# Kernel optimization log

Hardware: AMD Instinct MI355X
Metric: run time of the kernel (lower is better)

Reference implementation:

```python
import jax, jax.numpy as jnp
import numpy as np

EPS = 1e-5
TEMP = 3.0
MASK_FILL = 1e-4


def _conv2d(x, w, b):
    # x: [N,C,H,W], w: [O,C,kh,kw], stride 1, padding 1
    y = jax.lax.conv_general_dilated(x, w, (1, 1), [(1, 1), (1, 1)],
                                     dimension_numbers=('NCHW', 'OIHW', 'NCHW'))
    return y + b[None, :, None, None]


def _cp_conv4d(x, w1, b1, w2, b2):
    # CenterPivotConv4d: 2D conv over (ha,wa) per (hb,wb) + 2D conv over (hb,wb) per (ha,wa)
    B, C, ha, wa, hb, wb = x.shape
    O = w1.shape[0]
    x1 = x.transpose(0, 4, 5, 1, 2, 3).reshape(B * hb * wb, C, ha, wa)
    o1 = _conv2d(x1, w1, b1).reshape(B, hb, wb, O, ha, wa).transpose(0, 3, 4, 5, 1, 2)
    x2 = x.transpose(0, 2, 3, 1, 4, 5).reshape(B * ha * wa, C, hb, wb)
    o2 = _conv2d(x2, w2, b2).reshape(B, ha, wa, O, hb, wb).transpose(0, 3, 1, 2, 4, 5)
    return o1 + o2


def _mutual_matching(c):
    # c: [B,ch,fs1,fs2,fs3,fs4]; corr * (corr/maxA) * (corr/maxB)
    mA = jnp.max(c, axis=(4, 5), keepdims=True)  # max over (fs3*fs4)
    mB = jnp.max(c, axis=(2, 3), keepdims=True)  # max over (fs1*fs2)
    return c * (c / (mA + EPS)) * (c / (mB + EPS))


def _neigh_consensus(x, params):
    def stack(y):
        for (w1, b1, w2, b2) in params:
            y = jax.nn.relu(_cp_conv4d(y, w1, b1, w2, b2))
        return y
    # symmetric mode: conv(x) + conv(x with pairs swapped) swapped back
    xp = x.transpose(0, 1, 4, 5, 2, 3)
    return stack(x) + stack(xp).transpose(0, 1, 4, 5, 2, 3)


def setup_inputs() -> dict:
    key = jax.random.key(0)
    ks = jax.random.split(key, 16)
    B, S, Cv = 4, 32, 256
    corr = jax.random.normal(ks[0], (B, S, S, S, S), dtype=jnp.float32)
    v = jax.random.normal(ks[1], (B, Cv, S * S), dtype=jnp.float32)
    ig_mask = jax.random.randint(ks[2], (B, S * S), 0, 2) > 0
    layer_io = [(1, 10), (10, 10), (10, 1)]
    inp = {'corr': corr, 'v': v, 'ig_mask': ig_mask}
    for i, (ci, co) in enumerate(layer_io):
        k1, k2 = jax.random.split(ks[3 + i])
        inp[f'l{i}_w1'] = jax.random.normal(k1, (co, ci, 3, 3), dtype=jnp.float32) * 0.1
        inp[f'l{i}_b1'] = jnp.zeros((co,), dtype=jnp.float32)
        inp[f'l{i}_w2'] = jax.random.normal(k2, (co, ci, 3, 3), dtype=jnp.float32) * 0.1
        inp[f'l{i}_b2'] = jnp.zeros((co,), dtype=jnp.float32)
    return inp


def reference(corr, v, ig_mask,
              l0_w1, l0_b1, l0_w2, l0_b2,
              l1_w1, l1_b1, l1_w2, l1_b2,
              l2_w1, l2_b1, l2_w2, l2_b2):
    params = [(l0_w1, l0_b1, l0_w2, l0_b2),
              (l1_w1, l1_b1, l1_w2, l1_b2),
              (l2_w1, l2_b1, l2_w2, l2_b2)]
    B, h, w, hs, ws = corr.shape
    c = corr[:, None]                      # [B,1,h,w,hs,ws]
    c = _mutual_matching(c)
    c = _neigh_consensus(c, params)
    c = _mutual_matching(c)
    corr2d = c.reshape(B, h * w, hs * ws)
    corr2d = jnp.where(ig_mask[:, None, :], MASK_FILL, corr2d)
    attn = jax.nn.softmax(corr2d * TEMP, axis=-1)  # [B, hw, hsws]
    weighted_v = jnp.einsum('bcs,bqs->bcq', v, attn)
    return weighted_v.reshape(B, -1, h, w)
```

## Files before the change

kernel.cpp:

```cpp
#include <hip/hip_runtime.h>
#include <math.h>

#define BN 4
#define HW 1024
#define SP 1024

static constexpr float EPS = 1e-5f;
static constexpr float TEMPF = 3.0f;
static constexpr float MASK_FILL = 1e-4f;
static constexpr size_t CH1 = (size_t)HW * SP;
static constexpr size_t CH10 = (size_t)10 * HW * SP;

__device__ __forceinline__ float wave_max(float v) {
    for (int o = 32; o; o >>= 1) v = fmaxf(v, __shfl_xor(v, o));
    return v;
}
__device__ __forceinline__ float wave_sum(float v) {
    for (int o = 32; o; o >>= 1) v += __shfl_xor(v, o);
    return v;
}
__device__ __forceinline__ float block_max(float v, float* red) {
    v = wave_max(v);
    int w = threadIdx.x >> 6;
    if ((threadIdx.x & 63) == 0) red[w] = v;
    __syncthreads();
    v = fmaxf(fmaxf(red[0], red[1]), fmaxf(red[2], red[3]));
    __syncthreads();
    return v;
}
__device__ __forceinline__ float block_sum(float v, float* red) {
    v = wave_sum(v);
    int w = threadIdx.x >> 6;
    if ((threadIdx.x & 63) == 0) red[w] = v;
    __syncthreads();
    v = red[0] + red[1] + red[2] + red[3];
    __syncthreads();
    return v;
}

__global__ void wt_prep(const float* __restrict__ l0w1, const float* __restrict__ l0w2,
                        const float* __restrict__ l1w1, const float* __restrict__ l1w2,
                        const float* __restrict__ l2w1, const float* __restrict__ l2w2,
                        float* __restrict__ wt) {
    int t = threadIdx.x;
    for (int i = t; i < 90; i += 256) {
        int co = i % 10, tap = i / 10;
        wt[tap * 20 + co] = l0w1[co * 9 + tap];
        wt[tap * 20 + 10 + co] = l0w2[co * 9 + tap];
    }
    for (int i = t; i < 900; i += 256) {
        int co = i % 10, tap = (i / 10) % 9, ci = i / 90;
        wt[180 + ci * 180 + tap * 20 + co] = l1w1[(co * 10 + ci) * 9 + tap];
        wt[180 + ci * 180 + tap * 20 + 10 + co] = l1w2[(co * 10 + ci) * 9 + tap];
    }
    for (int i = t; i < 90; i += 256) {
        int tap = i % 9, ci = i / 9;
        wt[1980 + ci * 18 + tap * 2 + 0] = l2w1[ci * 9 + tap];
        wt[1980 + ci * 18 + tap * 2 + 1] = l2w2[ci * 9 + tap];
    }
}

template <bool SUM2>
__global__ void colmax_part(const float* __restrict__ in1, const float* __restrict__ in2,
                            float* __restrict__ part) {
    size_t b = blockIdx.y;
    in1 += b * CH1; in2 += b * CH1; part += b * 256 * SP;
    int blk = blockIdx.x;
    int p4 = threadIdx.x << 2;
    size_t base = (size_t)blk * 4 * SP + p4;
    float4 m = {-INFINITY, -INFINITY, -INFINITY, -INFINITY};
#pragma unroll
    for (int r = 0; r < 4; ++r) {
        float4 v = *(const float4*)&in1[base + (size_t)r * SP];
        if (SUM2) {
            float4 u = *(const float4*)&in2[base + (size_t)r * SP];
            v.x += u.x; v.y += u.y; v.z += u.z; v.w += u.w;
        }
        m.x = fmaxf(m.x, v.x); m.y = fmaxf(m.y, v.y);
        m.z = fmaxf(m.z, v.z); m.w = fmaxf(m.w, v.w);
    }
    *(float4*)&part[(size_t)blk * SP + p4] = m;
}

__global__ void colmax_comb(const float* __restrict__ part, float* __restrict__ binv) {
    size_t b = blockIdx.y;
    part += b * 256 * SP; binv += b * SP;
    int col = (blockIdx.x << 8) + threadIdx.x;
    float m = -INFINITY;
    for (int c = 0; c < 256; ++c) m = fmaxf(m, part[(size_t)c * SP + col]);
    binv[col] = 1.0f / (m + EPS);
}

__global__ void mm_rows(const float* __restrict__ in, const float* __restrict__ binv,
                        float* __restrict__ out) {
    size_t b = blockIdx.y;
    in += b * CH1; binv += b * SP; out += b * CH1;
    __shared__ float red[4];
    int row = blockIdx.x;
    int p4 = threadIdx.x << 2;
    float4 v = *(const float4*)&in[(size_t)row * SP + p4];
    float m = fmaxf(fmaxf(v.x, v.y), fmaxf(v.z, v.w));
    m = block_max(m, red);
    float rinv = 1.0f / (m + EPS);
    float4 bi = *(const float4*)&binv[p4];
    float4 o;
    o.x = v.x * v.x * v.x * rinv * bi.x;
    o.y = v.y * v.y * v.y * rinv * bi.y;
    o.z = v.z * v.z * v.z * rinv * bi.z;
    o.w = v.w * v.w * v.w * rinv * bi.w;
    *(float4*)&out[(size_t)row * SP + p4] = o;
}

template <int CI, int CO, bool SWAP>
__device__ __forceinline__ void conv_body(const float* __restrict__ in,
                                          float* __restrict__ out,
                                          const float* __restrict__ wt,
                                          const float* __restrict__ bA,
                                          const float* __restrict__ bB,
                                          float (*tile)[SP], int hw) {
    int h = hw >> 5, w = hw & 31;
    int tid = threadIdx.x;
    int p4 = tid << 2;
    int ws0 = p4 & 31;
    int hs = p4 >> 5;

    float acc[CO][4];
#pragma unroll
    for (int co = 0; co < CO; ++co) {
        float bsum = bA[co] + bB[co];
#pragma unroll
        for (int k = 0; k < 4; ++k) acc[co][k] = bsum;
    }

    float4 pre = *(const float4*)&in[(size_t)hw * SP + p4];
    for (int ci = 0; ci < CI; ++ci) {
        const float* wci = wt + ci * 9 * 2 * CO;
        float* tl = tile[ci & 1];
        *(float4*)&tl[p4] = pre;
        __syncthreads();
        if (ci + 1 < CI)
            pre = *(const float4*)&in[((size_t)(ci + 1) * HW + hw) * SP + p4];
        const float* inc = in + (size_t)ci * HW * SP;
#pragma unroll
        for (int dh = -1; dh <= 1; ++dh) {
            bool hok = (unsigned)(h + dh) < 32u;
            bool v2 = (unsigned)(hs + dh) < 32u;
            int b2 = p4 + dh * 32;
            float4 c4 = {0.f, 0.f, 0.f, 0.f};
            if (v2) c4 = *(const float4*)&tl[b2];
            float lm = (v2 && ws0 > 0) ? tl[b2 - 1] : 0.0f;
            float lp = (v2 && ws0 < 28) ? tl[b2 + 4] : 0.0f;
            float4 l4[3];
            l4[0] = {lm, c4.x, c4.y, c4.z};
            l4[1] = c4;
            l4[2] = {c4.y, c4.z, c4.w, lp};
#pragma unroll
            for (int dwi = 0; dwi < 3; ++dwi) {
                int dw = dwi - 1;
                bool v1 = hok && ((unsigned)(w + dw) < 32u);
                float4 g4 = {0.f, 0.f, 0.f, 0.f};
                if (v1) g4 = *(const float4*)&inc[(size_t)(hw + dh * 32 + dw) * SP + p4];
                int tap = (dh + 1) * 3 + dwi;
                const float* wp = wci + tap * 2 * CO;
                if constexpr (CO == 10) {
                    float4 f0 = *(const float4*)&wp[0];
                    float4 f1 = *(const float4*)&wp[4];
                    float4 f2 = *(const float4*)&wp[8];
                    float4 f3 = *(const float4*)&wp[12];
                    float4 f4 = *(const float4*)&wp[16];
                    float wa[10] = {f0.x, f0.y, f0.z, f0.w, f1.x,
                                    f1.y, f1.z, f1.w, f2.x, f2.y};
                    float wb[10] = {f2.z, f2.w, f3.x, f3.y, f3.z,
                                    f3.w, f4.x, f4.y, f4.z, f4.w};
#pragma unroll
                    for (int co = 0; co < 10; ++co) {
                        float w1v = SWAP ? wb[co] : wa[co];
                        float w2v = SWAP ? wa[co] : wb[co];
                        acc[co][0] = fmaf(g4.x, w1v, fmaf(l4[dwi].x, w2v, acc[co][0]));
                        acc[co][1] = fmaf(g4.y, w1v, fmaf(l4[dwi].y, w2v, acc[co][1]));
                        acc[co][2] = fmaf(g4.z, w1v, fmaf(l4[dwi].z, w2v, acc[co][2]));
                        acc[co][3] = fmaf(g4.w, w1v, fmaf(l4[dwi].w, w2v, acc[co][3]));
                    }
                } else {
                    float2 f = *(const float2*)&wp[0];
                    float w1v = SWAP ? f.y : f.x;
                    float w2v = SWAP ? f.x : f.y;
                    acc[0][0] = fmaf(g4.x, w1v, fmaf(l4[dwi].x, w2v, acc[0][0]));
                    acc[0][1] = fmaf(g4.y, w1v, fmaf(l4[dwi].y, w2v, acc[0][1]));
                    acc[0][2] = fmaf(g4.z, w1v, fmaf(l4[dwi].z, w2v, acc[0][2]));
                    acc[0][3] = fmaf(g4.w, w1v, fmaf(l4[dwi].w, w2v, acc[0][3]));
                }
            }
        }
        __syncthreads();
    }

#pragma unroll
    for (int co = 0; co < CO; ++co) {
        float* op = out + ((size_t)co * HW + hw) * SP + p4;
        float4 r;
        r.x = fmaxf(acc[co][0], 0.0f);
        r.y = fmaxf(acc[co][1], 0.0f);
        r.z = fmaxf(acc[co][2], 0.0f);
        r.w = fmaxf(acc[co][3], 0.0f);
        *(float4*)op = r;
    }
}

template <int CI, int CO>
__global__ __launch_bounds__(256) void conv4d(
    const float* __restrict__ in0, const float* __restrict__ in1,
    float* __restrict__ out0, float* __restrict__ out1,
    const float* __restrict__ wt,
    const float* __restrict__ bA, const float* __restrict__ bB,
    int branch_base) {
    __shared__ float tile[2][SP];
    int branch = blockIdx.y + branch_base;
    int hw = blockIdx.x;
    if (branch == 0)
        conv_body<CI, CO, false>(in0, out0, wt, bA, bB, tile, hw);
    else
        conv_body<CI, CO, true>(in1, out1, wt, bA, bB, tile, hw);
}

__global__ void mm_softmax(const float* __restrict__ s1, const float* __restrict__ s2,
                           const float* __restrict__ binv, const int* __restrict__ mask,
                           float* __restrict__ attn) {
    size_t b = blockIdx.y;
    s1 += b * CH1; s2 += b * CH1; binv += b * SP; mask += b * SP; attn += b * CH1;
    __shared__ float red[4];
    int row = blockIdx.x;
    int p4 = threadIdx.x << 2;
    float4 v = *(const float4*)&s1[(size_t)row * SP + p4];
    float4 u = *(const float4*)&s2[(size_t)row * SP + p4];
    v.x += u.x; v.y += u.y; v.z += u.z; v.w += u.w;
    float m = fmaxf(fmaxf(v.x, v.y), fmaxf(v.z, v.w));
    m = block_max(m, red);
    float rinv = 1.0f / (m + EPS);
    float4 bi = *(const float4*)&binv[p4];
    int4 mk = *(const int4*)&mask[p4];
    float lg[4];
    lg[0] = (mk.x != 0) ? MASK_FILL * TEMPF : v.x * v.x * v.x * rinv * bi.x * TEMPF;
    lg[1] = (mk.y != 0) ? MASK_FILL * TEMPF : v.y * v.y * v.y * rinv * bi.y * TEMPF;
    lg[2] = (mk.z != 0) ? MASK_FILL * TEMPF : v.z * v.z * v.z * rinv * bi.z * TEMPF;
    lg[3] = (mk.w != 0) ? MASK_FILL * TEMPF : v.w * v.w * v.w * rinv * bi.w * TEMPF;
    float lm = fmaxf(fmaxf(lg[0], lg[1]), fmaxf(lg[2], lg[3]));
    lm = block_max(lm, red);
    float e[4], ss = 0.0f;
#pragma unroll
    for (int k = 0; k < 4; ++k) {
        e[k] = expf(lg[k] - lm);
        ss += e[k];
    }
    ss = block_sum(ss, red);
    float inv = 1.0f / ss;
    float4 o = {e[0] * inv, e[1] * inv, e[2] * inv, e[3] * inv};
    *(float4*)&attn[(size_t)row * SP + p4] = o;
}

__global__ __launch_bounds__(256) void gemm_vat(const float* __restrict__ V,
                                                const float* __restrict__ A,
                                                float* __restrict__ out) {
    size_t b = blockIdx.z;
    V += b * 256 * 1024; A += b * CH1; out += b * 256 * 1024;
    __shared__ float As[64][36];
    __shared__ float Bs[64][36];
    int c0 = blockIdx.y * 64, q0 = blockIdx.x * 64;
    int tr = threadIdx.x & 15, tc = threadIdx.x >> 4;
    float acc[4][4] = {};
    for (int k0 = 0; k0 < 1024; k0 += 32) {
#pragma unroll
        for (int j = 0; j < 2; ++j) {
            int idx = threadIdx.x + j * 256;
            int row = idx >> 3, c4 = (idx & 7) * 4;
            *(float4*)&As[row][c4] = *(const float4*)&V[(size_t)(c0 + row) * 1024 + k0 + c4];
            *(float4*)&Bs[row][c4] = *(const float4*)&A[(size_t)(q0 + row) * 1024 + k0 + c4];
        }
        __syncthreads();
#pragma unroll
        for (int kk = 0; kk < 8; ++kk) {
            float4 a[4], bb[4];
#pragma unroll
            for (int i = 0; i < 4; ++i) a[i] = *(float4*)&As[tr * 4 + i][kk * 4];
#pragma unroll
            for (int j = 0; j < 4; ++j) bb[j] = *(float4*)&Bs[tc * 4 + j][kk * 4];
#pragma unroll
            for (int i = 0; i < 4; ++i)
#pragma unroll
                for (int j = 0; j < 4; ++j)
                    acc[i][j] += a[i].x * bb[j].x + a[i].y * bb[j].y +
                                 a[i].z * bb[j].z + a[i].w * bb[j].w;
        }
        __syncthreads();
    }
#pragma unroll
    for (int i = 0; i < 4; ++i) {
        float4 o = {acc[i][0], acc[i][1], acc[i][2], acc[i][3]};
        *(float4*)&out[(size_t)(c0 + tr * 4 + i) * 1024 + q0 + tc * 4] = o;
    }
}

extern "C" void kernel_launch(void* const* d_in, const int* in_sizes, int n_in,
                              void* d_out, int out_size, void* d_ws, size_t ws_size,
                              hipStream_t stream) {
    const float* corr = (const float*)d_in[0];
    const float* v = (const float*)d_in[1];
    const int* mask = (const int*)d_in[2];
    const float* l0w1 = (const float*)d_in[3];
    const float* l0b1 = (const float*)d_in[4];
    const float* l0w2 = (const float*)d_in[5];
    const float* l0b2 = (const float*)d_in[6];
    const float* l1w1 = (const float*)d_in[7];
    const float* l1b1 = (const float*)d_in[8];
    const float* l1w2 = (const float*)d_in[9];
    const float* l1b2 = (const float*)d_in[10];
    const float* l2w1 = (const float*)d_in[11];
    const float* l2b1 = (const float*)d_in[12];
    const float* l2w2 = (const float*)d_in[13];
    const float* l2b2 = (const float*)d_in[14];
    float* W = (float*)d_ws;
    float* out = (float*)d_out;
    (void)in_sizes; (void)n_in; (void)out_size;

    const size_t need2 = (4 * CH10 + 12 * CH1 + 2160) * sizeof(float);
    const size_t need1 = (4 * CH10 + 2 * CH1 + 2160) * sizeof(float);
    dim3 g2(HW, 2), g1(HW, 1);

    if (ws_size >= need2) {
        float* P1 = W;
        float* Q1 = P1 + CH10;
        float* P2 = Q1 + CH10;
        float* Q2 = P2 + CH10;
        float* C1 = Q2 + CH10;
        float* S = C1 + 4 * CH1;
        float* wt = S + 8 * CH1;
        float* PART = P2;
        float* MB0 = P2 + 4 * 256 * SP;
        float* MB1 = MB0 + 4 * SP;
        float* ATTN = P1;

        wt_prep<<<1, 256, 0, stream>>>(l0w1, l0w2, l1w1, l1w2, l2w1, l2w2, wt);

        colmax_part<false><<<dim3(256, BN), 256, 0, stream>>>(corr, corr, PART);
        colmax_comb<<<dim3(4, BN), 256, 0, stream>>>(PART, MB0);
        mm_rows<<<dim3(HW, BN), 256, 0, stream>>>(corr, MB0, C1);

        for (int b = 0; b < BN; ++b) {
            float* C1b = C1 + (size_t)b * CH1;
            float* S1b = S + (size_t)b * CH1;
            float* S2b = S + (size_t)(4 + b) * CH1;
            conv4d<1, 10><<<g2, 256, 0, stream>>>(C1b, C1b, P1, P2, wt, l0b1, l0b2, 0);
            conv4d<10, 10><<<g2, 256, 0, stream>>>(P1, P2, Q1, Q2, wt + 180, l1b1, l1b2, 0);
            conv4d<10, 1><<<g2, 256, 0, stream>>>(Q1, Q2, S1b, S2b, wt + 1980, l2b1, l2b2, 0);
        }

        colmax_part<true><<<dim3(256, BN), 256, 0, stream>>>(S, S + 4 * CH1, PART);
        colmax_comb<<<dim3(4, BN), 256, 0, stream>>>(PART, MB1);
        mm_softmax<<<dim3(HW, BN), 256, 0, stream>>>(S, S + 4 * CH1, MB1, mask, ATTN);
        gemm_vat<<<dim3(16, 4, BN), 256, 0, stream>>>(v, ATTN, out);
    } else {
        bool par = ws_size >= need1;
        float *P1, *Q1, *P2, *Q2, *C1, *S1, *S2, *wt;
        if (par) {
            P1 = W; Q1 = P1 + CH10; P2 = Q1 + CH10; Q2 = P2 + CH10;
            S1 = Q2 + CH10; S2 = S1 + CH1; wt = S2 + CH1;
            C1 = Q1;
        } else {
            P1 = W; Q1 = P1 + CH10; C1 = Q1 + CH10; S1 = C1 + CH1; S2 = S1 + CH1;
            wt = S2 + CH1;
            P2 = P1; Q2 = Q1;
        }
        float* PART = P1;
        float* MB0 = P1 + 256 * SP;
        float* MB1 = MB0 + SP;
        float* ATTN = P1 + 512 * SP;

        wt_prep<<<1, 256, 0, stream>>>(l0w1, l0w2, l1w1, l1w2, l2w1, l2w2, wt);

        for (int b = 0; b < BN; ++b) {
            const float* corr_b = corr + (size_t)b * CH1;
            const float* v_b = v + (size_t)b * 256 * 1024;
            const int* mask_b = mask + (size_t)b * SP;
            float* out_b = out + (size_t)b * 256 * 1024;

            colmax_part<false><<<dim3(256, 1), 256, 0, stream>>>(corr_b, corr_b, PART);
            colmax_comb<<<dim3(4, 1), 256, 0, stream>>>(PART, MB0);
            mm_rows<<<dim3(HW, 1), 256, 0, stream>>>(corr_b, MB0, C1);

            if (par) {
                conv4d<1, 10><<<g2, 256, 0, stream>>>(C1, C1, P1, P2, wt, l0b1, l0b2, 0);
                conv4d<10, 10><<<g2, 256, 0, stream>>>(P1, P2, Q1, Q2, wt + 180, l1b1, l1b2, 0);
                conv4d<10, 1><<<g2, 256, 0, stream>>>(Q1, Q2, S1, S2, wt + 1980, l2b1, l2b2, 0);
            } else {
                conv4d<1, 10><<<g1, 256, 0, stream>>>(C1, C1, P1, P1, wt, l0b1, l0b2, 0);
                conv4d<10, 10><<<g1, 256, 0, stream>>>(P1, P1, Q1, Q1, wt + 180, l1b1, l1b2, 0);
                conv4d<10, 1><<<g1, 256, 0, stream>>>(Q1, Q1, S1, S1, wt + 1980, l2b1, l2b2, 0);
                conv4d<1, 10><<<g1, 256, 0, stream>>>(C1, C1, P1, P1, wt, l0b1, l0b2, 1);
                conv4d<10, 10><<<g1, 256, 0, stream>>>(P1, P1, Q1, Q1, wt + 180, l1b1, l1b2, 1);
                conv4d<10, 1><<<g1, 256, 0, stream>>>(Q1, Q1, S2, S2, wt + 1980, l2b1, l2b2, 1);
            }

            colmax_part<true><<<dim3(256, 1), 256, 0, stream>>>(S1, S2, PART);
            colmax_comb<<<dim3(4, 1), 256, 0, stream>>>(PART, MB1);
            mm_softmax<<<dim3(HW, 1), 256, 0, stream>>>(S1, S2, MB1, mask_b, ATTN);
            gemm_vat<<<dim3(16, 4, 1), 256, 0, stream>>>(v_b, ATTN, out_b);
        }
    }
}
```

Measured before the change: 909.1 us.

## Process two adjacent (h,w) positions per block in the 10-to-10 conv layer

Adds a conv4d_pair kernel for the middle 10-channel CenterPivot conv layer in which each block computes two neighbouring w positions instead of one. The global loads of neighbouring rows along w are shared between the two outputs (4 loads instead of 6 per dh), and the grid is halved. In exchange, per-thread accumulators double to 80 floats and shared memory doubles, which raises register pressure and may reduce occupancy.

Result: faster. 869.4 us (-4.4%).

```diff
diff --git a/kernel.cpp b/kernel.cpp
--- a/kernel.cpp
+++ b/kernel.cpp
@@ -221,6 +221,126 @@
         conv_body<CI, CO, false>(in0, out0, wt, bA, bB, tile, hw);
     else
         conv_body<CI, CO, true>(in1, out1, wt, bA, bB, tile, hw);
+}
+
+template <bool SWAP>
+__device__ __forceinline__ void conv_pair_body(const float* __restrict__ in,
+                                               float* __restrict__ out,
+                                               const float* __restrict__ wt,
+                                               const float* __restrict__ bA,
+                                               const float* __restrict__ bB,
+                                               float (*tile)[2][SP], int h, int w0) {
+    int tid = threadIdx.x;
+    int p4 = tid << 2;
+    int ws0 = p4 & 31;
+    int hs = p4 >> 5;
+    int hw0 = h * 32 + w0;
+
+    float acc0[10][4], acc1[10][4];
+#pragma unroll
+    for (int co = 0; co < 10; ++co) {
+        float bsum = bA[co] + bB[co];
+#pragma unroll
+        for (int k = 0; k < 4; ++k) { acc0[co][k] = bsum; acc1[co][k] = bsum; }
+    }
+
+    float4 preA = *(const float4*)&in[(size_t)hw0 * SP + p4];
+    float4 preB = *(const float4*)&in[(size_t)(hw0 + 1) * SP + p4];
+    for (int ci = 0; ci < 10; ++ci) {
+        const float* wci = wt + ci * 180;
+        float* tlA = tile[ci & 1][0];
+        float* tlB = tile[ci & 1][1];
+        *(float4*)&tlA[p4] = preA;
+        *(float4*)&tlB[p4] = preB;
+        __syncthreads();
+        if (ci + 1 < 10) {
+            preA = *(const float4*)&in[((size_t)(ci + 1) * HW + hw0) * SP + p4];
+            preB = *(const float4*)&in[((size_t)(ci + 1) * HW + hw0 + 1) * SP + p4];
+        }
+        const float* inc = in + (size_t)ci * HW * SP;
+#pragma unroll
+        for (int dh = -1; dh <= 1; ++dh) {
+            bool hok = (unsigned)(h + dh) < 32u;
+            bool v2 = (unsigned)(hs + dh) < 32u;
+            int b2 = p4 + dh * 32;
+            float4 cA = {0.f, 0.f, 0.f, 0.f}, cB = {0.f, 0.f, 0.f, 0.f};
+            float lmA = 0.f, lpA = 0.f, lmB = 0.f, lpB = 0.f;
+            if (v2) {
+                cA = *(const float4*)&tlA[b2];
+                cB = *(const float4*)&tlB[b2];
+                if (ws0 > 0) { lmA = tlA[b2 - 1]; lmB = tlB[b2 - 1]; }
+                if (ws0 < 28) { lpA = tlA[b2 + 4]; lpB = tlB[b2 + 4]; }
+            }
+            float4 lA[3], lB[3];
+            lA[0] = {lmA, cA.x, cA.y, cA.z}; lA[1] = cA; lA[2] = {cA.y, cA.z, cA.w, lpA};
+            lB[0] = {lmB, cB.x, cB.y, cB.z}; lB[1] = cB; lB[2] = {cB.y, cB.z, cB.w, lpB};
+            float4 g[4];
+#pragma unroll
+            for (int dc = 0; dc < 4; ++dc) {
+                bool ok = hok && ((unsigned)(w0 + dc - 1) < 32u);
+                g[dc] = {0.f, 0.f, 0.f, 0.f};
+                if (ok) g[dc] = *(const float4*)&inc[(size_t)(hw0 + dh * 32 + dc - 1) * SP + p4];
+            }
+#pragma unroll
+            for (int dwi = 0; dwi < 3; ++dwi) {
+                int tap = (dh + 1) * 3 + dwi;
+                const float* wp = wci + tap * 20;
+                float4 f0 = *(const float4*)&wp[0];
+                float4 f1 = *(const float4*)&wp[4];
+                float4 f2 = *(const float4*)&wp[8];
+                float4 f3 = *(const float4*)&wp[12];
+                float4 f4 = *(const float4*)&wp[16];
+                float wa[10] = {f0.x, f0.y, f0.z, f0.w, f1.x,
+                                f1.y, f1.z, f1.w, f2.x, f2.y};
+                float wb[10] = {f2.z, f2.w, f3.x, f3.y, f3.z,
+                                f3.w, f4.x, f4.y, f4.z, f4.w};
+#pragma unroll
+                for (int co = 0; co < 10; ++co) {
+                    float w1v = SWAP ? wb[co] : wa[co];
+                    float w2v = SWAP ? wa[co] : wb[co];
+                    acc0[co][0] = fmaf(g[dwi].x, w1v, fmaf(lA[dwi].x, w2v, acc0[co][0]));
+                    acc0[co][1] = fmaf(g[dwi].y, w1v, fmaf(lA[dwi].y, w2v, acc0[co][1]));
+                    acc0[co][2] = fmaf(g[dwi].z, w1v, fmaf(lA[dwi].z, w2v, acc0[co][2]));
+                    acc0[co][3] = fmaf(g[dwi].w, w1v, fmaf(lA[dwi].w, w2v, acc0[co][3]));
+                    acc1[co][0] = fmaf(g[dwi + 1].x, w1v, fmaf(lB[dwi].x, w2v, acc1[co][0]));
+                    acc1[co][1] = fmaf(g[dwi + 1].y, w1v, fmaf(lB[dwi].y, w2v, acc1[co][1]));
+                    acc1[co][2] = fmaf(g[dwi + 1].z, w1v, fmaf(lB[dwi].z, w2v, acc1[co][2]));
+                    acc1[co][3] = fmaf(g[dwi + 1].w, w1v, fmaf(lB[dwi].w, w2v, acc1[co][3]));
+                }
+            }
+        }
+        __syncthreads();
+    }
+
+#pragma unroll
+    for (int co = 0; co < 10; ++co) {
+        float* op0 = out + ((size_t)co * HW + hw0) * SP + p4;
+        float* op1 = op0 + SP;
+        float4 r0, r1;
+        r0.x = fmaxf(acc0[co][0], 0.0f); r0.y = fmaxf(acc0[co][1], 0.0f);
+        r0.z = fmaxf(acc0[co][2], 0.0f); r0.w = fmaxf(acc0[co][3], 0.0f);
+        r1.x = fmaxf(acc1[co][0], 0.0f); r1.y = fmaxf(acc1[co][1], 0.0f);
+        r1.z = fmaxf(acc1[co][2], 0.0f); r1.w = fmaxf(acc1[co][3], 0.0f);
+        *(float4*)op0 = r0;
+        *(float4*)op1 = r1;
+    }
+}
+
+__global__ __launch_bounds__(256) void conv4d_pair(
+    const float* __restrict__ in0, const float* __restrict__ in1,
+    float* __restrict__ out0, float* __restrict__ out1,
+    const float* __restrict__ wt,
+    const float* __restrict__ bA, const float* __restrict__ bB,
+    int branch_base) {
+    __shared__ float tile[2][2][SP];
+    int branch = blockIdx.y + branch_base;
+    int bx = blockIdx.x;
+    int h = bx >> 4;
+    int w0 = (bx & 15) << 1;
+    if (branch == 0)
+        conv_pair_body<false>(in0, out0, wt, bA, bB, tile, h, w0);
+    else
+        conv_pair_body<true>(in1, out1, wt, bA, bB, tile, h, w0);
 }
 
 __global__ void mm_softmax(const float* __restrict__ s1, const float* __restrict__ s2,
@@ -325,6 +445,7 @@
     const size_t need2 = (4 * CH10 + 12 * CH1 + 2160) * sizeof(float);
     const size_t need1 = (4 * CH10 + 2 * CH1 + 2160) * sizeof(float);
     dim3 g2(HW, 2), g1(HW, 1);
+    dim3 gp2(512, 2), gp1(512, 1);
 
     if (ws_size >= need2) {
         float* P1 = W;
@@ -350,7 +471,7 @@
             float* S1b = S + (size_t)b * CH1;
             float* S2b = S + (size_t)(4 + b) * CH1;
             conv4d<1, 10><<<g2, 256, 0, stream>>>(C1b, C1b, P1, P2, wt, l0b1, l0b2, 0);
-            conv4d<10, 10><<<g2, 256, 0, stream>>>(P1, P2, Q1, Q2, wt + 180, l1b1, l1b2, 0);
+            conv4d_pair<<<gp2, 256, 0, stream>>>(P1, P2, Q1, Q2, wt + 180, l1b1, l1b2, 0);
             conv4d<10, 1><<<g2, 256, 0, stream>>>(Q1, Q2, S1b, S2b, wt + 1980, l2b1, l2b2, 0);
         }
 
@@ -389,14 +510,14 @@
 
             if (par) {
                 conv4d<1, 10><<<g2, 256, 0, stream>>>(C1, C1, P1, P2, wt, l0b1, l0b2, 0);
-                conv4d<10, 10><<<g2, 256, 0, stream>>>(P1, P2, Q1, Q2, wt + 180, l1b1, l1b2, 0);
+                conv4d_pair<<<gp2, 256, 0, stream>>>(P1, P2, Q1, Q2, wt + 180, l1b1, l1b2, 0);
                 conv4d<10, 1><<<g2, 256, 0, stream>>>(Q1, Q2, S1, S2, wt + 1980, l2b1, l2b2, 0);
             } else {
                 conv4d<1, 10><<<g1, 256, 0, stream>>>(C1, C1, P1, P1, wt, l0b1, l0b2, 0);
-                conv4d<10, 10><<<g1, 256, 0, stream>>>(P1, P1, Q1, Q1, wt + 180, l1b1, l1b2, 0);
+                conv4d_pair<<<gp1, 256, 0, stream>>>(P1, P1, Q1, Q1, wt + 180, l1b1, l1b2, 0);
                 conv4d<10, 1><<<g1, 256, 0, stream>>>(Q1, Q1, S1, S1, wt + 1980, l2b1, l2b2, 0);
                 conv4d<1, 10><<<g1, 256, 0, stream>>>(C1, C1, P1, P1, wt, l0b1, l0b2, 1);
-                conv4d<10, 10><<<g1, 256, 0, stream>>>(P1, P1, Q1, Q1, wt + 180, l1b1, l1b2, 1);
+                conv4d_pair<<<gp1, 256, 0, stream>>>(P1, P1, Q1, Q1, wt + 180, l1b1, l1b2, 1);
                 conv4d<10, 1><<<g1, 256, 0, stream>>>(Q1, Q1, S2, S2, wt + 1980, l2b1, l2b2, 1);
             }
 
```

## Compute two adjacent output columns per conv4d block to share loads

Applied to the files above, without the earlier changes.

Each block of the conv4d kernel now produces two neighbouring (h,w) output positions instead of one. The overlapping gathered inputs along w are shared, so each dh step issues 4 global loads instead of 6, and the weight loads are reused across both outputs. The trailing per-iteration barrier is dropped and the double-buffered shared tile is relied on for safety. In exchange the block count is halved and accumulator register pressure doubles, which may reduce occupancy.

After: 836.1 us, median of 2. 1.09x faster.

```diff
diff --git a/kernel.cpp b/kernel.cpp
--- a/kernel.cpp
+++ b/kernel.cpp
@@ -112,54 +112,65 @@
 }
 
 template <int CI, int CO, bool SWAP>
-__device__ __forceinline__ void conv_body(const float* __restrict__ in,
-                                          float* __restrict__ out,
-                                          const float* __restrict__ wt,
-                                          const float* __restrict__ bA,
-                                          const float* __restrict__ bB,
-                                          float (*tile)[SP], int hw) {
-    int h = hw >> 5, w = hw & 31;
+__device__ __forceinline__ void conv_pair_body(const float* __restrict__ in,
+                                               float* __restrict__ out,
+                                               const float* __restrict__ wt,
+                                               const float* __restrict__ bA,
+                                               const float* __restrict__ bB,
+                                               float (*tile)[2][SP], int h, int w0) {
     int tid = threadIdx.x;
     int p4 = tid << 2;
     int ws0 = p4 & 31;
     int hs = p4 >> 5;
-
-    float acc[CO][4];
+    int hw0 = h * 32 + w0;
+
+    float acc0[CO][4], acc1[CO][4];
 #pragma unroll
     for (int co = 0; co < CO; ++co) {
         float bsum = bA[co] + bB[co];
 #pragma unroll
-        for (int k = 0; k < 4; ++k) acc[co][k] = bsum;
-    }
-
-    float4 pre = *(const float4*)&in[(size_t)hw * SP + p4];
+        for (int k = 0; k < 4; ++k) { acc0[co][k] = bsum; acc1[co][k] = bsum; }
+    }
+
+    float4 preA = *(const float4*)&in[(size_t)hw0 * SP + p4];
+    float4 preB = *(const float4*)&in[(size_t)(hw0 + 1) * SP + p4];
     for (int ci = 0; ci < CI; ++ci) {
         const float* wci = wt + ci * 9 * 2 * CO;
-        float* tl = tile[ci & 1];
-        *(float4*)&tl[p4] = pre;
+        float* tlA = tile[ci & 1][0];
+        float* tlB = tile[ci & 1][1];
+        *(float4*)&tlA[p4] = preA;
+        *(float4*)&tlB[p4] = preB;
         __syncthreads();
-        if (ci + 1 < CI)
-            pre = *(const float4*)&in[((size_t)(ci + 1) * HW + hw) * SP + p4];
+        if (ci + 1 < CI) {
+            preA = *(const float4*)&in[((size_t)(ci + 1) * HW + hw0) * SP + p4];
+            preB = *(const float4*)&in[((size_t)(ci + 1) * HW + hw0 + 1) * SP + p4];
+        }
         const float* inc = in + (size_t)ci * HW * SP;
 #pragma unroll
         for (int dh = -1; dh <= 1; ++dh) {
             bool hok = (unsigned)(h + dh) < 32u;
             bool v2 = (unsigned)(hs + dh) < 32u;
             int b2 = p4 + dh * 32;
-            float4 c4 = {0.f, 0.f, 0.f, 0.f};
-            if (v2) c4 = *(const float4*)&tl[b2];
-            float lm = (v2 && ws0 > 0) ? tl[b2 - 1] : 0.0f;
-            float lp = (v2 && ws0 < 28) ? tl[b2 + 4] : 0.0f;
-            float4 l4[3];
-            l4[0] = {lm, c4.x, c4.y, c4.z};
-            l4[1] = c4;
-            l4[2] = {c4.y, c4.z, c4.w, lp};
+            float4 cA = {0.f, 0.f, 0.f, 0.f}, cB = {0.f, 0.f, 0.f, 0.f};
+            float lmA = 0.f, lpA = 0.f, lmB = 0.f, lpB = 0.f;
+            if (v2) {
+                cA = *(const float4*)&tlA[b2];
+                cB = *(const float4*)&tlB[b2];
+                if (ws0 > 0) { lmA = tlA[b2 - 1]; lmB = tlB[b2 - 1]; }
+                if (ws0 < 28) { lpA = tlA[b2 + 4]; lpB = tlB[b2 + 4]; }
+            }
+            float4 lA[3], lB[3];
+            lA[0] = {lmA, cA.x, cA.y, cA.z}; lA[1] = cA; lA[2] = {cA.y, cA.z, cA.w, lpA};
+            lB[0] = {lmB, cB.x, cB.y, cB.z}; lB[1] = cB; lB[2] = {cB.y, cB.z, cB.w, lpB};
+            float4 g[4];
+#pragma unroll
+            for (int dc = 0; dc < 4; ++dc) {
+                bool ok = hok && ((unsigned)(w0 + dc - 1) < 32u);
+                g[dc] = {0.f, 0.f, 0.f, 0.f};
+                if (ok) g[dc] = *(const float4*)&inc[(size_t)(hw0 + dh * 32 + dc - 1) * SP + p4];
+            }
 #pragma unroll
             for (int dwi = 0; dwi < 3; ++dwi) {
-                int dw = dwi - 1;
-                bool v1 = hok && ((unsigned)(w + dw) < 32u);
-                float4 g4 = {0.f, 0.f, 0.f, 0.f};
-                if (v1) g4 = *(const float4*)&inc[(size_t)(hw + dh * 32 + dw) * SP + p4];
                 int tap = (dh + 1) * 3 + dwi;
                 const float* wp = wci + tap * 2 * CO;
                 if constexpr (CO == 10) {
@@ -176,51 +187,62 @@
                     for (int co = 0; co < 10; ++co) {
                         float w1v = SWAP ? wb[co] : wa[co];
                         float w2v = SWAP ? wa[co] : wb[co];
-                        acc[co][0] = fmaf(g4.x, w1v, fmaf(l4[dwi].x, w2v, acc[co][0]));
-                        acc[co][1] = fmaf(g4.y, w1v, fmaf(l4[dwi].y, w2v, acc[co][1]));
-                        acc[co][2] = fmaf(g4.z, w1v, fmaf(l4[dwi].z, w2v, acc[co][2]));
-                        acc[co][3] = fmaf(g4.w, w1v, fmaf(l4[dwi].w, w2v, acc[co][3]));
+                        acc0[co][0] = fmaf(g[dwi].x, w1v, fmaf(lA[dwi].x, w2v, acc0[co][0]));
+                        acc0[co][1] = fmaf(g[dwi].y, w1v, fmaf(lA[dwi].y, w2v, acc0[co][1]));
+                        acc0[co][2] = fmaf(g[dwi].z, w1v, fmaf(lA[dwi].z, w2v, acc0[co][2]));
+                        acc0[co][3] = fmaf(g[dwi].w, w1v, fmaf(lA[dwi].w, w2v, acc0[co][3]));
+                        acc1[co][0] = fmaf(g[dwi + 1].x, w1v, fmaf(lB[dwi].x, w2v, acc1[co][0]));
+                        acc1[co][1] = fmaf(g[dwi + 1].y, w1v, fmaf(lB[dwi].y, w2v, acc1[co][1]));
+                        acc1[co][2] = fmaf(g[dwi + 1].z, w1v, fmaf(lB[dwi].z, w2v, acc1[co][2]));
+                        acc1[co][3] = fmaf(g[dwi + 1].w, w1v, fmaf(lB[dwi].w, w2v, acc1[co][3]));
                     }
                 } else {
                     float2 f = *(const float2*)&wp[0];
                     float w1v = SWAP ? f.y : f.x;
                     float w2v = SWAP ? f.x : f.y;
-                    acc[0][0] = fmaf(g4.x, w1v, fmaf(l4[dwi].x, w2v, acc[0][0]));
-                    acc[0][1] = fmaf(g4.y, w1v, fmaf(l4[dwi].y, w2v, acc[0][1]));
-                    acc[0][2] = fmaf(g4.z, w1v, fmaf(l4[dwi].z, w2v, acc[0][2]));
-                    acc[0][3] = fmaf(g4.w, w1v, fmaf(l4[dwi].w, w2v, acc[0][3]));
+                    acc0[0][0] = fmaf(g[dwi].x, w1v, fmaf(lA[dwi].x, w2v, acc0[0][0]));
+                    acc0[0][1] = fmaf(g[dwi].y, w1v, fmaf(lA[dwi].y, w2v, acc0[0][1]));
+                    acc0[0][2] = fmaf(g[dwi].z, w1v, fmaf(lA[dwi].z, w2v, acc0[0][2]));
+                    acc0[0][3] = fmaf(g[dwi].w, w1v, fmaf(lA[dwi].w, w2v, acc0[0][3]));
+                    acc1[0][0] = fmaf(g[dwi + 1].x, w1v, fmaf(lB[dwi].x, w2v, acc1[0][0]));
+                    acc1[0][1] = fmaf(g[dwi + 1].y, w1v, fmaf(lB[dwi].y, w2v, acc1[0][1]));
+                    acc1[0][2] = fmaf(g[dwi + 1].z, w1v, fmaf(lB[dwi].z, w2v, acc1[0][2]));
+                    acc1[0][3] = fmaf(g[dwi + 1].w, w1v, fmaf(lB[dwi].w, w2v, acc1[0][3]));
                 }
             }
         }
-        __syncthreads();
     }
 
 #pragma unroll
     for (int co = 0; co < CO; ++co) {
-        float* op = out + ((size_t)co * HW + hw) * SP + p4;
-        float4 r;
-        r.x = fmaxf(acc[co][0], 0.0f);
-        r.y = fmaxf(acc[co][1], 0.0f);
-        r.z = fmaxf(acc[co][2], 0.0f);
-        r.w = fmaxf(acc[co][3], 0.0f);
-        *(float4*)op = r;
+        float* op0 = out + ((size_t)co * HW + hw0) * SP + p4;
+        float* op1 = op0 + SP;
+        float4 r0, r1;
+        r0.x = fmaxf(acc0[co][0], 0.0f); r0.y = fmaxf(acc0[co][1], 0.0f);
+        r0.z = fmaxf(acc0[co][2], 0.0f); r0.w = fmaxf(acc0[co][3], 0.0f);
+        r1.x = fmaxf(acc1[co][0], 0.0f); r1.y = fmaxf(acc1[co][1], 0.0f);
+        r1.z = fmaxf(acc1[co][2], 0.0f); r1.w = fmaxf(acc1[co][3], 0.0f);
+        *(float4*)op0 = r0;
+        *(float4*)op1 = r1;
     }
 }
 
 template <int CI, int CO>
-__global__ __launch_bounds__(256) void conv4d(
+__global__ __launch_bounds__(256) void conv4d_pair(
     const float* __restrict__ in0, const float* __restrict__ in1,
     float* __restrict__ out0, float* __restrict__ out1,
     const float* __restrict__ wt,
     const float* __restrict__ bA, const float* __restrict__ bB,
     int branch_base) {
-    __shared__ float tile[2][SP];
+    __shared__ float tile[2][2][SP];
     int branch = blockIdx.y + branch_base;
-    int hw = blockIdx.x;
+    int bx = blockIdx.x;
+    int h = bx >> 4;
+    int w0 = (bx & 15) << 1;
     if (branch == 0)
-        conv_body<CI, CO, false>(in0, out0, wt, bA, bB, tile, hw);
+        conv_pair_body<CI, CO, false>(in0, out0, wt, bA, bB, tile, h, w0);
     else
-        conv_body<CI, CO, true>(in1, out1, wt, bA, bB, tile, hw);
+        conv_pair_body<CI, CO, true>(in1, out1, wt, bA, bB, tile, h, w0);
 }
 
 __global__ void mm_softmax(const float* __restrict__ s1, const float* __restrict__ s2,
@@ -324,7 +346,7 @@
 
     const size_t need2 = (4 * CH10 + 12 * CH1 + 2160) * sizeof(float);
     const size_t need1 = (4 * CH10 + 2 * CH1 + 2160) * sizeof(float);
-    dim3 g2(HW, 2), g1(HW, 1);
+    dim3 gp2(512, 2), gp1(512, 1);
 
     if (ws_size >= need2) {
         float* P1 = W;
@@ -349,9 +371,9 @@
             float* C1b = C1 + (size_t)b * CH1;
             float* S1b = S + (size_t)b * CH1;
             float* S2b = S + (size_t)(4 + b) * CH1;
-            conv4d<1, 10><<<g2, 256, 0, stream>>>(C1b, C1b, P1, P2, wt, l0b1, l0b2, 0);
-            conv4d<10, 10><<<g2, 256, 0, stream>>>(P1, P2, Q1, Q2, wt + 180, l1b1, l1b2, 0);
-            conv4d<10, 1><<<g2, 256, 0, stream>>>(Q1, Q2, S1b, S2b, wt + 1980, l2b1, l2b2, 0);
+            conv4d_pair<1, 10><<<gp2, 256, 0, stream>>>(C1b, C1b, P1, P2, wt, l0b1, l0b2, 0);
+            conv4d_pair<10, 10><<<gp2, 256, 0, stream>>>(P1, P2, Q1, Q2, wt + 180, l1b1, l1b2, 0);
+            conv4d_pair<10, 1><<<gp2, 256, 0, stream>>>(Q1, Q2, S1b, S2b, wt + 1980, l2b1, l2b2, 0);
         }
 
         colmax_part<true><<<dim3(256, BN), 256, 0, stream>>>(S, S + 4 * CH1, PART);
@@ -388,16 +410,16 @@
             mm_rows<<<dim3(HW, 1), 256, 0, stream>>>(corr_b, MB0, C1);
 
             if (par) {
-                conv4d<1, 10><<<g2, 256, 0, stream>>>(C1, C1, P1, P2, wt, l0b1, l0b2, 0);
-                conv4d<10, 10><<<g2, 256, 0, stream>>>(P1, P2, Q1, Q2, wt + 180, l1b1, l1b2, 0);
-                conv4d<10, 1><<<g2, 256, 0, stream>>>(Q1, Q2, S1, S2, wt + 1980, l2b1, l2b2, 0);
+                conv4d_pair<1, 10><<<gp2, 256, 0, stream>>>(C1, C1, P1, P2, wt, l0b1, l0b2, 0);
+                conv4d_pair<10, 10><<<gp2, 256, 0, stream>>>(P1, P2, Q1, Q2, wt + 180, l1b1, l1b2, 0);
+                conv4d_pair<10, 1><<<gp2, 256, 0, stream>>>(Q1, Q2, S1, S2, wt + 1980, l2b1, l2b2, 0);
             } else {
-                conv4d<1, 10><<<g1, 256, 0, stream>>>(C1, C1, P1, P1, wt, l0b1, l0b2, 0);
-                conv4d<10, 10><<<g1, 256, 0, stream>>>(P1, P1, Q1, Q1, wt + 180, l1b1, l1b2, 0);
-                conv4d<10, 1><<<g1, 256, 0, stream>>>(Q1, Q1, S1, S1, wt + 1980, l2b1, l2b2, 0);
-                conv4d<1, 10><<<g1, 256, 0, stream>>>(C1, C1, P1, P1, wt, l0b1, l0b2, 1);
-                conv4d<10, 10><<<g1, 256, 0, stream>>>(P1, P1, Q1, Q1, wt + 180, l1b1, l1b2, 1);
-                conv4d<10, 1><<<g1, 256, 0, stream>>>(Q1, Q1, S2, S2, wt + 1980, l2b1, l2b2, 1);
+                conv4d_pair<1, 10><<<gp1, 256, 0, stream>>>(C1, C1, P1, P1, wt, l0b1, l0b2, 0);
+                conv4d_pair<10, 10><<<gp1, 256, 0, stream>>>(P1, P1, Q1, Q1, wt + 180, l1b1, l1b2, 0);
+                conv4d_pair<10, 1><<<gp1, 256, 0, stream>>>(Q1, Q1, S1, S1, wt + 1980, l2b1, l2b2, 0);
+                conv4d_pair<1, 10><<<gp1, 256, 0, stream>>>(C1, C1, P1, P1, wt, l0b1, l0b2, 1);
+                conv4d_pair<10, 10><<<gp1, 256, 0, stream>>>(P1, P1, Q1, Q1, wt + 180, l1b1, l1b2, 1);
+                conv4d_pair<10, 1><<<gp1, 256, 0, stream>>>(Q1, Q1, S2, S2, wt + 1980, l2b1, l2b2, 1);
             }
 
             colmax_part<true><<<dim3(256, 1), 256, 0, stream>>>(S1, S2, PART);
```
